# Kernel tuning notes

Hardware: AMD Instinct MI355X
Metric: run time of the kernel (lower is better)

Reference implementation:

```python
import jax, jax.numpy as jnp
import numpy as np

D_MODEL = 2048
N_HEAD = 16
SEM_DIM = 1024
GEO_DIM = 1024
ATTN_DIM = 2048
ROPE_BASE = 10000.0


def _rope(x, base=ROPE_BASE):
    # x: [B, H, S, d] with even d; GPT-NeoX rotate-half convention
    S, d = x.shape[-2], x.shape[-1]
    inv_freq = 1.0 / (base ** (jnp.arange(0, d, 2, dtype=jnp.float32) / d))
    t = jnp.arange(S, dtype=jnp.float32)
    freqs = jnp.einsum('s,f->sf', t, inv_freq)  # [S, d/2]
    cos, sin = jnp.cos(freqs), jnp.sin(freqs)
    x1, x2 = x[..., : d // 2], x[..., d // 2 :]
    return jnp.concatenate([x1 * cos - x2 * sin, x1 * sin + x2 * cos], axis=-1).astype(x.dtype)


def _split_heads(y, H):
    B, S, dim = y.shape
    return y.reshape(B, S, H, dim // H).transpose(0, 2, 1, 3)  # [B,H,S,hd]


def setup_inputs() -> dict:
    key = jax.random.key(0)
    ks = jax.random.split(key, 7)
    B, S = 2, 2048
    sd = 0.02
    return {
        'x': jax.random.normal(ks[0], (B, S, D_MODEL), dtype=jnp.float32),
        'Wq_sem': jax.random.normal(ks[1], (SEM_DIM, D_MODEL), dtype=jnp.float32) * sd,
        'Wk_sem': jax.random.normal(ks[2], (SEM_DIM, D_MODEL), dtype=jnp.float32) * sd,
        'Wq_geo': jax.random.normal(ks[3], (GEO_DIM, D_MODEL), dtype=jnp.float32) * sd,
        'Wk_geo': jax.random.normal(ks[4], (GEO_DIM, D_MODEL), dtype=jnp.float32) * sd,
        'Wv': jax.random.normal(ks[5], (ATTN_DIM, D_MODEL), dtype=jnp.float32) * sd,
        'Wo': jax.random.normal(ks[6], (D_MODEL, ATTN_DIM), dtype=jnp.float32) * sd,
    }


def reference(x, Wq_sem, Wk_sem, Wq_geo, Wk_geo, Wv, Wo):
    B, S, _ = x.shape
    H = N_HEAD
    # decoupled projections (nn.Linear: y = x @ W.T)
    q_sem = _split_heads(x @ Wq_sem.T, H)  # [B,H,S,64]
    k_sem = _split_heads(x @ Wk_sem.T, H)
    q_geo = _rope(_split_heads(x @ Wq_geo.T, H))  # RoPE only on geo part
    k_geo = _rope(_split_heads(x @ Wk_geo.T, H))
    v = _split_heads(x @ Wv.T, H)  # [B,H,S,128]
    # concatenated decoupled q/k -> single fused score (fp32), SDPA default scale
    q = jnp.concatenate([q_sem, q_geo], axis=-1)
    k = jnp.concatenate([k_sem, k_geo], axis=-1)
    scale = 1.0 / jnp.sqrt(jnp.asarray(q.shape[-1], dtype=jnp.float32))
    scores = jnp.einsum('bhqd,bhkd->bhqk', q, k).astype(jnp.float32) * scale
    causal = jnp.tril(jnp.ones((S, S), dtype=bool))
    scores = jnp.where(causal, scores, jnp.finfo(jnp.float32).min)
    attn = jax.nn.softmax(scores, axis=-1).astype(v.dtype)
    out = jnp.einsum('bhqk,bhkd->bhqd', attn, v)  # [B,H,S,128]
    out = out.transpose(0, 2, 1, 3).reshape(B, S, ATTN_DIM)
    return out @ Wo.T  # [B,S,d_model]
```

## Files before the change

### kernel.cpp

```cpp
#include <hip/hip_runtime.h>
#include <cstdint>
#include <cstddef>

typedef unsigned short u16;
typedef __attribute__((ext_vector_type(8))) short bf16x8;
typedef __attribute__((ext_vector_type(4))) float f32x4;

#define MFMA32(a, b, c) __builtin_amdgcn_mfma_f32_16x16x32_bf16(a, b, c, 0, 0, 0)

__device__ __forceinline__ u16 f2b(float f) {
  union { float f; unsigned u; } v; v.f = f;
  unsigned u = v.u;
  return (u16)((u + 0x7fffu + ((u >> 16) & 1u)) >> 16);
}
__device__ __forceinline__ float b2f(u16 h) {
  union { unsigned u; float f; } v; v.u = ((unsigned)h) << 16;
  return v.f;
}

__device__ __forceinline__ void g2l16(const void* g, void* l) {
  __builtin_amdgcn_global_load_lds((__attribute__((address_space(1))) void*)(g),
                                   (__attribute__((address_space(3))) void*)(l), 16, 0, 0);
}

__global__ __launch_bounds__(256) void cast_all(const float* __restrict__ x,
                                                const float* __restrict__ W0,
                                                const float* __restrict__ W1,
                                                const float* __restrict__ W2,
                                                const float* __restrict__ W3,
                                                const float* __restrict__ Wv,
                                                const float* __restrict__ Wo,
                                                u16* __restrict__ xb,
                                                u16* __restrict__ Wall,
                                                u16* __restrict__ Wob) {
  const int blk = blockIdx.x;
  const float* src;
  u16* dst;
  int li;
  if (blk < 8192) {
    src = x; dst = xb; li = blk * 256 + threadIdx.x;
  } else if (blk < 16384) {
    const int s = (blk - 8192) >> 11;
    src = s == 0 ? W0 : s == 1 ? W1 : s == 2 ? W2 : W3;
    dst = Wall + (size_t)s * 2097152;
    li = ((blk - 8192) & 2047) * 256 + threadIdx.x;
  } else if (blk < 20480) {
    src = Wv; dst = Wall + (size_t)4 * 2097152;
    li = (blk - 16384) * 256 + threadIdx.x;
  } else {
    src = Wo; dst = Wob;
    li = (blk - 20480) * 256 + threadIdx.x;
  }
  float4 v = ((const float4*)src)[li];
  ushort4 r;
  r.x = f2b(v.x); r.y = f2b(v.y); r.z = f2b(v.z); r.w = f2b(v.w);
  ((ushort4*)dst)[li] = r;
}

template <bool BF16_OUT>
__global__ __launch_bounds__(256) void gemm_bt(const u16* __restrict__ A,
                                               const u16* __restrict__ B,
                                               void* __restrict__ C, int N, int K) {
  __shared__ u16 As[128 * 64];
  __shared__ u16 Bs[128 * 64];
  const int tid = threadIdx.x;
  const int wid = tid >> 6;
  const int lane = tid & 63;
  const int lm = lane & 15;
  const int quad = lane >> 4;
  const int r3 = lm & 7;
  const int wm = (wid & 1) * 64;
  const int wn = (wid >> 1) * 64;
  const int bm = blockIdx.y * 128;
  const int bn = blockIdx.x * 128;

  const u16* Ab = A + (size_t)bm * K;
  const u16* Bb = B + (size_t)bn * K;

  f32x4 zero = {0.f, 0.f, 0.f, 0.f};
  f32x4 acc[4][4];
#pragma unroll
  for (int i = 0; i < 4; ++i)
#pragma unroll
    for (int j = 0; j < 4; ++j) acc[i][j] = zero;

  for (int k0 = 0; k0 < K; k0 += 64) {
#pragma unroll
    for (int it = 0; it < 4; ++it) {
      int c = it * 256 + tid;
      int rg = c >> 6, rw = (c >> 3) & 7, u = c & 7;
      int row = rg * 8 + rw;
      int chd = u ^ rw;
      g2l16(Ab + (size_t)row * K + k0 + chd * 8, As + c * 8);
      g2l16(Bb + (size_t)row * K + k0 + chd * 8, Bs + c * 8);
    }
    __syncthreads();
#pragma unroll
    for (int ks = 0; ks < 2; ++ks) {
      bf16x8 a[4], b[4];
      int chd = ks * 4 + quad;
#pragma unroll
      for (int i = 0; i < 4; ++i) {
        int row = wm + i * 16 + lm;
        a[i] = *(const bf16x8*)(As + (((row >> 3) * 64 + r3 * 8 + (chd ^ r3)) * 8));
      }
#pragma unroll
      for (int j = 0; j < 4; ++j) {
        int row = wn + j * 16 + lm;
        b[j] = *(const bf16x8*)(Bs + (((row >> 3) * 64 + r3 * 8 + (chd ^ r3)) * 8));
      }
#pragma unroll
      for (int i = 0; i < 4; ++i)
#pragma unroll
        for (int j = 0; j < 4; ++j)
          acc[i][j] = MFMA32(a[i], b[j], acc[i][j]);
    }
    __syncthreads();
  }

#pragma unroll
  for (int i = 0; i < 4; ++i)
#pragma unroll
    for (int j = 0; j < 4; ++j)
#pragma unroll
      for (int r = 0; r < 4; ++r) {
        int row = bm + wm + i * 16 + quad * 4 + r;
        int col = bn + wn + j * 16 + lm;
        float v = acc[i][j][r];
        if (BF16_OUT)
          ((u16*)C)[(size_t)row * N + col] = f2b(v);
        else
          ((float*)C)[(size_t)row * N + col] = v;
      }
}

__global__ __launch_bounds__(512, 2) void gemm_qkv8(const u16* __restrict__ A,
                                                    const u16* __restrict__ B,
                                                    u16* __restrict__ Qb,
                                                    u16* __restrict__ Kb,
                                                    u16* __restrict__ VT) {
  constexpr int K = 2048;
  const float SC = 0.12751744f;
  extern __shared__ u16 sh[];
  u16* sA = sh;
  u16* sB = sh + 16384;
  const int tid = threadIdx.x;
  const int wid = tid >> 6, lane = tid & 63;
  const int lm = lane & 15, quad = lane >> 4, rx = lm & 7;
  const int wm = (wid >> 2) * 64;
  const int wn = (wid & 3) * 64;
  const int bm = blockIdx.y * 128;
  const int bn = blockIdx.x * 256;
  const u16* Ablk = A + (size_t)bm * K;
  const u16* Bblk = B + (size_t)bn * K;

  f32x4 zero = {0.f, 0.f, 0.f, 0.f};
  f32x4 acc[4][4];
#pragma unroll
  for (int i = 0; i < 4; ++i)
#pragma unroll
    for (int j = 0; j < 4; ++j) acc[i][j] = zero;

  bf16x8 aA[2][2];
  bf16x8 bB[2][2][2];

  auto stageu = [&](int st, int ut) {
    const int k0 = st << 6;
    const int bf = st & 1;
    const u16* src;
    u16* dst;
    int rowbase;
    if (ut == 0) { src = Ablk; rowbase = 0; dst = sA + bf * 8192; }
    else { src = Bblk; rowbase = (ut - 1) << 7; dst = sB + bf * 16384 + ((ut - 1) << 13); }
#pragma unroll
    for (int it = 0; it < 2; ++it) {
      const int c = it * 512 + tid;
      const int r = c >> 3, u = c & 7;
      g2l16(src + (size_t)(rowbase + r) * K + k0 + ((u ^ (r & 7)) << 3), dst + (size_t)c * 8);
    }
  };
  auto ldA = [&](int bf, int mh) {
    const u16* base = sA + bf * 8192;
#pragma unroll
    for (int ii = 0; ii < 2; ++ii)
#pragma unroll
      for (int ks = 0; ks < 2; ++ks) {
        const int row = wm + mh * 32 + ii * 16 + lm;
        aA[ii][ks] = *(const bf16x8*)(base + ((row * 8 + ((ks * 4 + quad) ^ rx)) << 3));
      }
  };
  auto ldB = [&](int bf, int nh) {
    const u16* base = sB + bf * 16384;
#pragma unroll
    for (int jj = 0; jj < 2; ++jj)
#pragma unroll
      for (int ks = 0; ks < 2; ++ks) {
        const int row = wn + nh * 32 + jj * 16 + lm;
        bB[nh][jj][ks] = *(const bf16x8*)(base + ((row * 8 + ((ks * 4 + quad) ^ rx)) << 3));
      }
  };
  auto mm = [&](int mh, int nh) {
    __builtin_amdgcn_s_setprio(1);
#pragma unroll
    for (int ii = 0; ii < 2; ++ii)
#pragma unroll
      for (int jj = 0; jj < 2; ++jj)
#pragma unroll
        for (int ks = 0; ks < 2; ++ks)
          acc[mh * 2 + ii][nh * 2 + jj] =
              MFMA32(aA[ii][ks], bB[nh][jj][ks], acc[mh * 2 + ii][nh * 2 + jj]);
    __builtin_amdgcn_s_setprio(0);
  };

  const int NT = K >> 6;
  const int NIT = NT >> 1;

  stageu(0, 0); stageu(0, 1); stageu(0, 2); stageu(1, 0);
  asm volatile("s_waitcnt vmcnt(2)" ::: "memory");
  __builtin_amdgcn_s_barrier();

#pragma unroll 1
  for (int i = 0; i < NIT; ++i) {
    const int t1 = 2 * i + 1, t2 = 2 * i + 2, t3 = 2 * i + 3;
    ldA(0, 0); ldB(0, 0);
    stageu(t1, 1);
    __builtin_amdgcn_s_barrier();
    mm(0, 0);
    __builtin_amdgcn_s_barrier();
    ldB(0, 1);
    stageu(t1, 2);
    __builtin_amdgcn_s_barrier();
    mm(0, 1);
    __builtin_amdgcn_s_barrier();
    ldA(0, 1);
    __builtin_amdgcn_s_barrier();
    mm(1, 1);
    __builtin_amdgcn_s_barrier();
    {
      const bool st = (t2 < NT);
      if (st) stageu(t2, 0);
      __builtin_amdgcn_s_barrier();
      mm(1, 0);
      if (st) asm volatile("s_waitcnt vmcnt(2)" ::: "memory");
      else    asm volatile("s_waitcnt vmcnt(0)" ::: "memory");
      __builtin_amdgcn_s_barrier();
    }
    ldA(1, 0); ldB(1, 0);
    if (t2 < NT) stageu(t2, 1);
    __builtin_amdgcn_s_barrier();
    mm(0, 0);
    __builtin_amdgcn_s_barrier();
    ldB(1, 1);
    if (t2 < NT) stageu(t2, 2);
    __builtin_amdgcn_s_barrier();
    mm(0, 1);
    __builtin_amdgcn_s_barrier();
    ldA(1, 1);
    __builtin_amdgcn_s_barrier();
    mm(1, 1);
    __builtin_amdgcn_s_barrier();
    {
      const bool st = (t3 < NT);
      if (st) stageu(t3, 0);
      __builtin_amdgcn_s_barrier();
      mm(1, 0);
      if (st) asm volatile("s_waitcnt vmcnt(2)" ::: "memory");
      else    asm volatile("s_waitcnt vmcnt(0)" ::: "memory");
      __builtin_amdgcn_s_barrier();
    }
  }

  const int seg = bn >> 10;
  const int b = bm >> 11;
  const int sbase = bm & 2047;
  const int h = ((bn + wn) >> 6) & 15;
  const size_t bhQ = (size_t)b * 16 + h;

  if (seg < 2) {
    u16* dst = (seg == 0) ? Qb : Kb;
    const float sc = (seg == 0) ? SC : 1.0f;
#pragma unroll
    for (int i = 0; i < 4; ++i)
#pragma unroll
      for (int r = 0; r < 4; ++r) {
        const int s = sbase + wm + i * 16 + quad * 4 + r;
        u16* base = dst + (bhQ * 2048 + s) * 128;
#pragma unroll
        for (int j = 0; j < 4; ++j) {
          const int d = (wn + j * 16 + lm) & 63;
          base[d] = f2b(acc[i][j][r] * sc);
        }
      }
  } else if (seg < 4) {
    u16* dst = (seg == 2) ? Qb : Kb;
    const float sc = (seg == 2) ? SC : 1.0f;
    const float inv0 = __powf(10000.0f, -(float)(2 * lm) * (1.0f / 64.0f));
    const float inv1 = __powf(10000.0f, -(float)(2 * (16 + lm)) * (1.0f / 64.0f));
#pragma unroll
    for (int i = 0; i < 4; ++i)
#pragma unroll
      for (int r = 0; r < 4; ++r) {
        const int s = sbase + wm + i * 16 + quad * 4 + r;
        float sn0, cs0, sn1, cs1;
        __sincosf((float)s * inv0, &sn0, &cs0);
        __sincosf((float)s * inv1, &sn1, &cs1);
        const float x1a = acc[i][0][r], x2a = acc[i][2][r];
        const float x1b = acc[i][1][r], x2b = acc[i][3][r];
        u16* base = dst + (bhQ * 2048 + s) * 128 + 64;
        base[lm]      = f2b((x1a * cs0 - x2a * sn0) * sc);
        base[16 + lm] = f2b((x1b * cs1 - x2b * sn1) * sc);
        base[32 + lm] = f2b((x1a * sn0 + x2a * cs0) * sc);
        base[48 + lm] = f2b((x1b * sn1 + x2b * cs1) * sc);
      }
  } else {
    const int hv0 = (bn - 4096) >> 7;
#pragma unroll
    for (int i = 0; i < 4; ++i)
#pragma unroll
      for (int r = 0; r < 4; ++r) {
        const int sr = wm + i * 16 + quad * 4 + r;
#pragma unroll
        for (int j = 0; j < 4; ++j) {
          const int d = wn + j * 16 + lm;
          sh[d * 128 + (((sr >> 3) ^ (d & 7)) << 3) + (sr & 7)] = f2b(acc[i][j][r]);
        }
      }
    __syncthreads();
#pragma unroll
    for (int it = 0; it < 8; ++it) {
      const int idx = it * 512 + tid;
      const int d = idx >> 4;
      const int ch = idx & 15;
      bf16x8 v = *(const bf16x8*)(sh + d * 128 + ((ch ^ (d & 7)) << 3));
      const size_t bh = (size_t)b * 16 + hv0 + (d >> 7);
      *(bf16x8*)(VT + (bh * 128 + (d & 127)) * 2048 + sbase + ch * 8) = v;
    }
  }
}

__global__ __launch_bounds__(256, 3) void attn_v9(const u16* __restrict__ Q,
                                                  const u16* __restrict__ K,
                                                  const u16* __restrict__ VT,
                                                  u16* __restrict__ O) {
  constexpr int S = 2048;
  constexpr int D = 128;
  __shared__ u16 Ks[64 * 128];
  __shared__ u16 Vs[128 * 64];
  __shared__ u16 Ps[64 * 72];
  const int linear = blockIdx.x + (blockIdx.y << 4);
  const int xcd = linear & 7;
  const int slot = linear >> 3;
  const int bh = (xcd << 2) + (slot >> 4);
  const int bx = slot & 15;
  const int b = bh >> 4, h = bh & 15;
  const int tid = threadIdx.x, wid = tid >> 6, lane = tid & 63;
  const int lm = lane & 15, quad = lane >> 4;
  const int rx = lm & 7;
  const int wrow = wid * 16;

  const u16* Kbh = K + (size_t)bh * S * D;
  const u16* Vbh = VT + (size_t)bh * D * S;

  const bf16x8 vones = {16256, 16256, 16256, 16256, 16256, 16256, 16256, 16256};

#pragma unroll 1
  for (int pass = 0; pass < 2; ++pass) {
    const int qt = pass == 0 ? bx : 31 - bx;

    bf16x8 aq[4];
#pragma unroll
    for (int ks = 0; ks < 4; ++ks)
      aq[ks] = *(const bf16x8*)(Q + ((size_t)bh * S + (size_t)qt * 64 + wrow + lm) * D +
                                ks * 32 + quad * 8);

    f32x4 zero = {0.f, 0.f, 0.f, 0.f};
    f32x4 lsum = zero;
    f32x4 oacc[8];
#pragma unroll
    for (int t = 0; t < 8; ++t) oacc[t] = zero;

#pragma unroll 1
    for (int kt = 0; kt <= qt; ++kt) {
      __syncthreads();
      const u16* Kt = Kbh + (size_t)kt * 64 * D;
      const u16* Vt = Vbh + (size_t)kt * 64;
#pragma unroll
      for (int it = 0; it < 4; ++it) {
        int c = it * 256 + tid;
        int row = c >> 4, u = c & 15;
        g2l16(Kt + (size_t)row * 128 + (size_t)(u ^ (row & 7)) * 8, Ks + c * 8);
      }
#pragma unroll
      for (int it = 0; it < 4; ++it) {
        int c = it * 256 + tid;
        int row = c >> 3, u = c & 7;
        g2l16(Vt + (size_t)row * S + (size_t)(u ^ (row & 7)) * 8, Vs + c * 8);
      }
      __syncthreads();

      f32x4 sc[4];
#pragma unroll
      for (int j = 0; j < 4; ++j) sc[j] = zero;
      __builtin_amdgcn_s_setprio(1);
#pragma unroll
      for (int ks = 0; ks < 4; ++ks) {
        const int kc = ks * 4 + quad;
#pragma unroll
        for (int j = 0; j < 4; ++j) {
          bf16x8 bk = *(const bf16x8*)(Ks + (((j * 16 + lm) * 16 + (kc ^ rx)) * 8));
          sc[j] = MFMA32(aq[ks], bk, sc[j]);
        }
      }
      __builtin_amdgcn_s_setprio(0);

      const bool diag = (kt == qt);
#pragma unroll
      for (int r = 0; r < 4; ++r) {
        const int qcol = wrow + quad * 4 + r;
        const int prow = (wrow + quad * 4 + r) * 72;
#pragma unroll
        for (int j = 0; j < 4; ++j) {
          float p = __builtin_amdgcn_exp2f(fminf(sc[j][r], 30.0f));
          if (diag && (j * 16 + lm > qcol)) p = 0.f;
          Ps[prow + j * 16 + lm] = f2b(p);
        }
      }

      __builtin_amdgcn_s_setprio(1);
#pragma unroll
      for (int ks = 0; ks < 2; ++ks) {
        bf16x8 ap = *(const bf16x8*)(Ps + (wrow + lm) * 72 + ks * 32 + quad * 8);
        const int kc = ks * 4 + quad;
        lsum = MFMA32(ap, vones, lsum);
#pragma unroll
        for (int t = 0; t < 8; ++t) {
          bf16x8 bv = *(const bf16x8*)(Vs + (((t * 16 + lm) * 8 + (kc ^ rx)) * 8));
          oacc[t] = MFMA32(ap, bv, oacc[t]);
        }
      }
      __builtin_amdgcn_s_setprio(0);
    }

#pragma unroll
    for (int r = 0; r < 4; ++r) {
      float inv = 1.0f / lsum[r];
      const int srow = qt * 64 + wrow + quad * 4 + r;
      u16* Orow = O + ((size_t)b * S + srow) * 2048 + h * 128;
#pragma unroll
      for (int t = 0; t < 8; ++t) Orow[t * 16 + lm] = f2b(oacc[t][r] * inv);
    }
  }
}

extern "C" void kernel_launch(void* const* d_in, const int* in_sizes, int n_in,
                              void* d_out, int out_size, void* d_ws, size_t ws_size,
                              hipStream_t stream) {
  const float* x      = (const float*)d_in[0];
  const float* Wq_sem = (const float*)d_in[1];
  const float* Wk_sem = (const float*)d_in[2];
  const float* Wq_geo = (const float*)d_in[3];
  const float* Wk_geo = (const float*)d_in[4];
  const float* Wv     = (const float*)d_in[5];
  const float* Wo     = (const float*)d_in[6];

  char* ws = (char*)d_ws;
  u16* xb   = (u16*)(ws);
  u16* Wall = (u16*)(ws + 16777216);
  u16* Wob  = (u16*)(ws + 16777216 + 25165824);
  u16* Qb   = (u16*)(ws + 16777216 + 25165824 + 8388608);
  u16* Ob   = Wall;
  u16* Kb   = (u16*)d_out;
  u16* VT   = (u16*)((char*)d_out + 16777216);

  hipFuncSetAttribute((const void*)gemm_qkv8,
                      hipFuncAttributeMaxDynamicSharedMemorySize, 98304);

  cast_all<<<24576, 256, 0, stream>>>(x, Wq_sem, Wk_sem, Wq_geo, Wk_geo, Wv, Wo,
                                      xb, Wall, Wob);

  gemm_qkv8<<<dim3(24, 32), 512, 98304, stream>>>(xb, Wall, Qb, Kb, VT);

  attn_v9<<<dim3(16, 32), 256, 0, stream>>>(Qb, Kb, VT, Ob);

  gemm_bt<false><<<dim3(16, 32), 256, 0, stream>>>(Ob, Wob, d_out, 2048, 2048);
}
```

Baseline: 338.4 us.

## Replace output projection GEMM with double-buffered 8-wave pipelined kernel

Swaps the simple single-buffered 128x128 gemm_bt for the output projection with a 512-thread, 128x256-tile kernel. The new kernel double-buffers LDS, interleaves async global-to-LDS staging with MFMA phases using barriers, and raises MFMA wave priority. It is meant to hide memory latency and increase per-block reuse in the final GEMM. In exchange it uses more LDS and launches fewer blocks (256), which may underfill the GPU's compute units.

```diff
diff --git a/kernel.cpp b/kernel.cpp
--- a/kernel.cpp
+++ b/kernel.cpp
@@ -57,83 +57,6 @@
   ((ushort4*)dst)[li] = r;
 }
 
-template <bool BF16_OUT>
-__global__ __launch_bounds__(256) void gemm_bt(const u16* __restrict__ A,
-                                               const u16* __restrict__ B,
-                                               void* __restrict__ C, int N, int K) {
-  __shared__ u16 As[128 * 64];
-  __shared__ u16 Bs[128 * 64];
-  const int tid = threadIdx.x;
-  const int wid = tid >> 6;
-  const int lane = tid & 63;
-  const int lm = lane & 15;
-  const int quad = lane >> 4;
-  const int r3 = lm & 7;
-  const int wm = (wid & 1) * 64;
-  const int wn = (wid >> 1) * 64;
-  const int bm = blockIdx.y * 128;
-  const int bn = blockIdx.x * 128;
-
-  const u16* Ab = A + (size_t)bm * K;
-  const u16* Bb = B + (size_t)bn * K;
-
-  f32x4 zero = {0.f, 0.f, 0.f, 0.f};
-  f32x4 acc[4][4];
-#pragma unroll
-  for (int i = 0; i < 4; ++i)
-#pragma unroll
-    for (int j = 0; j < 4; ++j) acc[i][j] = zero;
-
-  for (int k0 = 0; k0 < K; k0 += 64) {
-#pragma unroll
-    for (int it = 0; it < 4; ++it) {
-      int c = it * 256 + tid;
-      int rg = c >> 6, rw = (c >> 3) & 7, u = c & 7;
-      int row = rg * 8 + rw;
-      int chd = u ^ rw;
-      g2l16(Ab + (size_t)row * K + k0 + chd * 8, As + c * 8);
-      g2l16(Bb + (size_t)row * K + k0 + chd * 8, Bs + c * 8);
-    }
-    __syncthreads();
-#pragma unroll
-    for (int ks = 0; ks < 2; ++ks) {
-      bf16x8 a[4], b[4];
-      int chd = ks * 4 + quad;
-#pragma unroll
-      for (int i = 0; i < 4; ++i) {
-        int row = wm + i * 16 + lm;
-        a[i] = *(const bf16x8*)(As + (((row >> 3) * 64 + r3 * 8 + (chd ^ r3)) * 8));
-      }
-#pragma unroll
-      for (int j = 0; j < 4; ++j) {
-        int row = wn + j * 16 + lm;
-        b[j] = *(const bf16x8*)(Bs + (((row >> 3) * 64 + r3 * 8 + (chd ^ r3)) * 8));
-      }
-#pragma unroll
-      for (int i = 0; i < 4; ++i)
-#pragma unroll
-        for (int j = 0; j < 4; ++j)
-          acc[i][j] = MFMA32(a[i], b[j], acc[i][j]);
-    }
-    __syncthreads();
-  }
-
-#pragma unroll
-  for (int i = 0; i < 4; ++i)
-#pragma unroll
-    for (int j = 0; j < 4; ++j)
-#pragma unroll
-      for (int r = 0; r < 4; ++r) {
-        int row = bm + wm + i * 16 + quad * 4 + r;
-        int col = bn + wn + j * 16 + lm;
-        float v = acc[i][j][r];
-        if (BF16_OUT)
-          ((u16*)C)[(size_t)row * N + col] = f2b(v);
-        else
-          ((float*)C)[(size_t)row * N + col] = v;
-      }
-}
-
 __global__ __launch_bounds__(512, 2) void gemm_qkv8(const u16* __restrict__ A,
                                                     const u16* __restrict__ B,
                                                     u16* __restrict__ Qb,
@@ -338,6 +261,152 @@
   }
 }
 
+__global__ __launch_bounds__(512, 2) void gemm_out8(const u16* __restrict__ A,
+                                                    const u16* __restrict__ B,
+                                                    float* __restrict__ C) {
+  constexpr int K = 2048;
+  constexpr int N = 2048;
+  extern __shared__ u16 sh[];
+  u16* sA = sh;
+  u16* sB = sh + 16384;
+  const int tid = threadIdx.x;
+  const int wid = tid >> 6, lane = tid & 63;
+  const int lm = lane & 15, quad = lane >> 4, rx = lm & 7;
+  const int wm = (wid >> 2) * 64;
+  const int wn = (wid & 3) * 64;
+  const int bm = blockIdx.y * 128;
+  const int bn = blockIdx.x * 256;
+  const u16* Ablk = A + (size_t)bm * K;
+  const u16* Bblk = B + (size_t)bn * K;
+
+  f32x4 zero = {0.f, 0.f, 0.f, 0.f};
+  f32x4 acc[4][4];
+#pragma unroll
+  for (int i = 0; i < 4; ++i)
+#pragma unroll
+    for (int j = 0; j < 4; ++j) acc[i][j] = zero;
+
+  bf16x8 aA[2][2];
+  bf16x8 bB[2][2][2];
+
+  auto stageu = [&](int st, int ut) {
+    const int k0 = st << 6;
+    const int bf = st & 1;
+    const u16* src;
+    u16* dst;
+    int rowbase;
+    if (ut == 0) { src = Ablk; rowbase = 0; dst = sA + bf * 8192; }
+    else { src = Bblk; rowbase = (ut - 1) << 7; dst = sB + bf * 16384 + ((ut - 1) << 13); }
+#pragma unroll
+    for (int it = 0; it < 2; ++it) {
+      const int c = it * 512 + tid;
+      const int r = c >> 3, u = c & 7;
+      g2l16(src + (size_t)(rowbase + r) * K + k0 + ((u ^ (r & 7)) << 3), dst + (size_t)c * 8);
+    }
+  };
+  auto ldA = [&](int bf, int mh) {
+    const u16* base = sA + bf * 8192;
+#pragma unroll
+    for (int ii = 0; ii < 2; ++ii)
+#pragma unroll
+      for (int ks = 0; ks < 2; ++ks) {
+        const int row = wm + mh * 32 + ii * 16 + lm;
+        aA[ii][ks] = *(const bf16x8*)(base + ((row * 8 + ((ks * 4 + quad) ^ rx)) << 3));
+      }
+  };
+  auto ldB = [&](int bf, int nh) {
+    const u16* base = sB + bf * 16384;
+#pragma unroll
+    for (int jj = 0; jj < 2; ++jj)
+#pragma unroll
+      for (int ks = 0; ks < 2; ++ks) {
+        const int row = wn + nh * 32 + jj * 16 + lm;
+        bB[nh][jj][ks] = *(const bf16x8*)(base + ((row * 8 + ((ks * 4 + quad) ^ rx)) << 3));
+      }
+  };
+  auto mm = [&](int mh, int nh) {
+    __builtin_amdgcn_s_setprio(1);
+#pragma unroll
+    for (int ii = 0; ii < 2; ++ii)
+#pragma unroll
+      for (int jj = 0; jj < 2; ++jj)
+#pragma unroll
+        for (int ks = 0; ks < 2; ++ks)
+          acc[mh * 2 + ii][nh * 2 + jj] =
+              MFMA32(aA[ii][ks], bB[nh][jj][ks], acc[mh * 2 + ii][nh * 2 + jj]);
+    __builtin_amdgcn_s_setprio(0);
+  };
+
+  const int NT = K >> 6;
+  const int NIT = NT >> 1;
+
+  stageu(0, 0); stageu(0, 1); stageu(0, 2); stageu(1, 0);
+  asm volatile("s_waitcnt vmcnt(2)" ::: "memory");
+  __builtin_amdgcn_s_barrier();
+
+#pragma unroll 1
+  for (int i = 0; i < NIT; ++i) {
+    const int t1 = 2 * i + 1, t2 = 2 * i + 2, t3 = 2 * i + 3;
+    ldA(0, 0); ldB(0, 0);
+    stageu(t1, 1);
+    __builtin_amdgcn_s_barrier();
+    mm(0, 0);
+    __builtin_amdgcn_s_barrier();
+    ldB(0, 1);
+    stageu(t1, 2);
+    __builtin_amdgcn_s_barrier();
+    mm(0, 1);
+    __builtin_amdgcn_s_barrier();
+    ldA(0, 1);
+    __builtin_amdgcn_s_barrier();
+    mm(1, 1);
+    __builtin_amdgcn_s_barrier();
+    {
+      const bool st = (t2 < NT);
+      if (st) stageu(t2, 0);
+      __builtin_amdgcn_s_barrier();
+      mm(1, 0);
+      if (st) asm volatile("s_waitcnt vmcnt(2)" ::: "memory");
+      else    asm volatile("s_waitcnt vmcnt(0)" ::: "memory");
+      __builtin_amdgcn_s_barrier();
+    }
+    ldA(1, 0); ldB(1, 0);
+    if (t2 < NT) stageu(t2, 1);
+    __builtin_amdgcn_s_barrier();
+    mm(0, 0);
+    __builtin_amdgcn_s_barrier();
+    ldB(1, 1);
+    if (t2 < NT) stageu(t2, 2);
+    __builtin_amdgcn_s_barrier();
+    mm(0, 1);
+    __builtin_amdgcn_s_barrier();
+    ldA(1, 1);
+    __builtin_amdgcn_s_barrier();
+    mm(1, 1);
+    __builtin_amdgcn_s_barrier();
+    {
+      const bool st = (t3 < NT);
+      if (st) stageu(t3, 0);
+      __builtin_amdgcn_s_barrier();
+      mm(1, 0);
+      if (st) asm volatile("s_waitcnt vmcnt(2)" ::: "memory");
+      else    asm volatile("s_waitcnt vmcnt(0)" ::: "memory");
+      __builtin_amdgcn_s_barrier();
+    }
+  }
+
+#pragma unroll
+  for (int i = 0; i < 4; ++i)
+#pragma unroll
+    for (int j = 0; j < 4; ++j)
+#pragma unroll
+      for (int r = 0; r < 4; ++r) {
+        const int row = bm + wm + i * 16 + quad * 4 + r;
+        const int col = bn + wn + j * 16 + lm;
+        C[(size_t)row * N + col] = acc[i][j][r];
+      }
+}
+
 __global__ __launch_bounds__(256, 3) void attn_v9(const u16* __restrict__ Q,
                                                   const u16* __restrict__ K,
                                                   const u16* __restrict__ VT,
@@ -474,6 +543,8 @@
 
   hipFuncSetAttribute((const void*)gemm_qkv8,
                       hipFuncAttributeMaxDynamicSharedMemorySize, 98304);
+  hipFuncSetAttribute((const void*)gemm_out8,
+                      hipFuncAttributeMaxDynamicSharedMemorySize, 98304);
 
   cast_all<<<24576, 256, 0, stream>>>(x, Wq_sem, Wk_sem, Wq_geo, Wk_geo, Wv, Wo,
                                       xb, Wall, Wob);
@@ -482,5 +553,5 @@
 
   attn_v9<<<dim3(16, 32), 256, 0, stream>>>(Qb, Kb, VT, Ob);
 
-  gemm_bt<false><<<dim3(16, 32), 256, 0, stream>>>(Ob, Wob, d_out, 2048, 2048);
-}
+  gemm_out8<<<dim3(8, 32), 512, 98304, stream>>>(Ob, Wob, (float*)d_out);
+}
```

After: 337.2 us. No clear change (-0.3%).
